# Optimization experiments

Measured on AMD Instinct MI355X. Metric: run time of the kernel, lower is better.

Reference implementation:

```python
import jax, jax.numpy as jnp
import numpy as np

N_NODES = 100000
N_EDGES = 1600000
N_GRAPHS = 2000
IN_DIM = 37
HID = 128
OUT_CLS = 2


def _leconv(x, src, dst, w, W1, b1, W2, W3, b3):
    # PyG LEConv: out[i] = sum_j w_ij * (lin1(x)[i] - lin2(x)[j]) + lin3(x)[i]
    a = x @ W1 + b1          # [N, H]
    b = x @ W2               # [N, H] (lin2 has no bias)
    c = x @ W3 + b3          # [N, H]
    deg = jax.ops.segment_sum(w, dst, num_segments=N_NODES)              # [N]
    agg = jax.ops.segment_sum(w[:, None] * b[src], dst, num_segments=N_NODES)  # [N, H]
    return deg[:, None] * a - agg + c


def setup_inputs() -> dict:
    key = jax.random.key(0)
    ks = jax.random.split(key, 32)
    inp = {}
    inp["x"] = jax.random.normal(ks[0], (N_NODES, IN_DIM), dtype=jnp.float32)
    inp["edge_index"] = jax.random.randint(ks[1], (2, N_EDGES), 0, N_NODES, dtype=jnp.int64)
    inp["batch"] = jnp.sort(jax.random.randint(ks[2], (N_NODES,), 0, N_GRAPHS, dtype=jnp.int64))
    dims = [(IN_DIM, HID), (HID, HID), (HID, HID)]
    ki = 3
    for l, (di, do) in enumerate(dims):
        s = 1.0 / np.sqrt(di)
        inp[f"W1_{l}"] = jax.random.uniform(ks[ki + 0], (di, do), jnp.float32, -s, s)
        inp[f"b1_{l}"] = jax.random.uniform(ks[ki + 1], (do,), jnp.float32, -s, s)
        inp[f"W2_{l}"] = jax.random.uniform(ks[ki + 2], (di, do), jnp.float32, -s, s)
        inp[f"W3_{l}"] = jax.random.uniform(ks[ki + 3], (di, do), jnp.float32, -s, s)
        inp[f"b3_{l}"] = jax.random.uniform(ks[ki + 4], (do,), jnp.float32, -s, s)
        ki += 5
    sf = 1.0 / np.sqrt(HID)
    inp["Wf1"] = jax.random.uniform(ks[ki + 0], (HID, HID), jnp.float32, -sf, sf)
    inp["bf1"] = jax.random.uniform(ks[ki + 1], (HID,), jnp.float32, -sf, sf)
    inp["Wf2"] = jax.random.uniform(ks[ki + 2], (HID, OUT_CLS), jnp.float32, -sf, sf)
    inp["bf2"] = jax.random.uniform(ks[ki + 3], (OUT_CLS,), jnp.float32, -sf, sf)
    return inp


def reference(x, edge_index, batch,
              W1_0, b1_0, W2_0, W3_0, b3_0,
              W1_1, b1_1, W2_1, W3_1, b3_1,
              W1_2, b1_2, W2_2, W3_2, b3_2,
              Wf1, bf1, Wf2, bf2):
    src, dst = edge_index[0], edge_index[1]
    w = jnp.ones((edge_index.shape[1],), dtype=x.dtype)  # edge_weight = ones
    layers = [(W1_0, b1_0, W2_0, W3_0, b3_0),
              (W1_1, b1_1, W2_1, W3_1, b3_1),
              (W1_2, b1_2, W2_2, W3_2, b3_2)]
    h = x
    for (W1, b1, W2, W3, b3) in layers:
        h = jax.nn.relu(_leconv(h, src, dst, w, W1, b1, W2, W3, b3))
    # global mean pool per graph
    sums = jax.ops.segment_sum(h, batch, num_segments=N_GRAPHS)           # [G, H]
    cnt = jax.ops.segment_sum(jnp.ones((N_NODES,), h.dtype), batch, num_segments=N_GRAPHS)
    graph_x = sums / jnp.clip(cnt, 1.0)[:, None]
    # FFN head (Dropout is identity at inference)
    pred = jax.nn.relu(graph_x @ Wf1 + bf1) @ Wf2 + bf2                   # [G, 2]
    return pred
```

## Files before the change

### kernel.cpp

```cpp
#include <hip/hip_runtime.h>
#include <hip/hip_bf16.h>
#include <cstdint>

#define N_NODES 100000
#define N_EDGES 1600000
#define N_GRAPHS 2000
#define IN_DIM 37
#define HID 128

#define GEMM_GRID 1563
#define HIST_BLOCKS 6250
#define PACK67_BLOCKS 384
#define PREPACK_BLOCKS 96

typedef __attribute__((ext_vector_type(8))) short short8;
typedef __attribute__((ext_vector_type(4))) float f32x4;

static __device__ __forceinline__ short bf16_bits(float f) {
    __hip_bfloat16 h = __float2bfloat16(f);
    return *reinterpret_cast<short*>(&h);
}
static __device__ __forceinline__ float bf16_lo(uint32_t u) {
    uint32_t v = u << 16;
    return *reinterpret_cast<float*>(&v);
}
static __device__ __forceinline__ float bf16_hi(uint32_t u) {
    uint32_t v = u & 0xffff0000u;
    return *reinterpret_cast<float*>(&v);
}


struct PackArgs {
    const float* w[9];
    short* o[9];
};

static __device__ __forceinline__ void pack_one(const PackArgs& pa, int m, int r, int kin) {
    const int i = r & 7, lane = (r >> 3) & 63, t = (r >> 9) & 7, kb = r >> 12;
    const int k = kb * 32 + (lane >> 4) * 8 + i;
    const int c = t * 16 + (lane & 15);
    float v = (k < kin) ? pa.w[m][(size_t)k * HID + c] : 0.f;
    pa.o[m][r] = bf16_bits(v);
}

__global__ __launch_bounds__(256) void prepack_kernel(PackArgs pa) {
    const int idx = blockIdx.x * 256 + threadIdx.x;
    pack_one(pa, idx >> 13, idx & 8191, IN_DIM);
}


static __device__ __forceinline__ void gemm0_body(
    int blk, const float* __restrict__ x,
    const short* __restrict__ Wp1, const short* __restrict__ Wp2, const short* __restrict__ Wp3,
    const float* __restrict__ b1v, const float* __restrict__ b3v,
    short* __restrict__ D0, short* __restrict__ E0, short* __restrict__ Bb) {
    const int tid = threadIdx.x;
    const int wave = tid >> 6, lane = tid & 63;
    const int row_base = blk * 64 + wave * 16;
    const int r15 = lane & 15, kg = lane >> 4;
    int arow = row_base + r15;
    if (arow >= N_NODES) arow = N_NODES - 1;
    const float* xr = x + (size_t)arow * IN_DIM;

    f32x4 acc1[8], acc2[8], acc3[8];
    #pragma unroll
    for (int t = 0; t < 8; t++) {
        acc1[t] = (f32x4)0.f; acc2[t] = (f32x4)0.f; acc3[t] = (f32x4)0.f;
    }
    #pragma unroll
    for (int kb = 0; kb < 2; kb++) {
        short8 av;
        #pragma unroll
        for (int i = 0; i < 8; i++) {
            const int k = kb * 32 + kg * 8 + i;
            av[i] = (k < IN_DIM) ? bf16_bits(xr[k]) : (short)0;
        }
        #pragma unroll
        for (int t = 0; t < 8; t++) {
            const int widx = (kb * 8 + t) * 512 + lane * 8;
            short8 w1 = *(const short8*)(Wp1 + widx);
            short8 w2 = *(const short8*)(Wp2 + widx);
            short8 w3 = *(const short8*)(Wp3 + widx);
            acc1[t] = __builtin_amdgcn_mfma_f32_16x16x32_bf16(av, w1, acc1[t], 0, 0, 0);
            acc2[t] = __builtin_amdgcn_mfma_f32_16x16x32_bf16(av, w2, acc2[t], 0, 0, 0);
            acc3[t] = __builtin_amdgcn_mfma_f32_16x16x32_bf16(av, w3, acc3[t], 0, 0, 0);
        }
    }
    int grow[4]; bool ok[4];
    #pragma unroll
    for (int i = 0; i < 4; i++) {
        grow[i] = row_base + kg * 4 + i;
        ok[i] = grow[i] < N_NODES;
    }
    #pragma unroll
    for (int t = 0; t < 8; t++) {
        const int c = t * 16 + r15;
        const float bb1 = b1v[c], bb3 = b3v[c];
        #pragma unroll
        for (int i = 0; i < 4; i++) {
            if (ok[i]) {
                size_t o = (size_t)grow[i] * HID + c;
                D0[o] = bf16_bits(acc1[t][i] + bb1);
                E0[o] = bf16_bits(acc3[t][i] + bb3);
                Bb[o] = bf16_bits(acc2[t][i]);
            }
        }
    }
}


struct P1Args {
    const float* x;
    const int* ei;
    int* cnt; int* rank;
    const short* Wp1; const short* Wp2; const short* Wp3;
    const float* b1; const float* b3;
    short* D0; short* E0; short* Bb;
    PackArgs pa;
};

__global__ __launch_bounds__(256) void phase1_kernel(P1Args a) {
    const int b = blockIdx.x;
    if (b < GEMM_GRID) {
        gemm0_body(b, a.x, a.Wp1, a.Wp2, a.Wp3, a.b1, a.b3, a.D0, a.E0, a.Bb);
        return;
    }
    if (b < GEMM_GRID + HIST_BLOCKS) {
        const int e = (b - GEMM_GRID) * 256 + threadIdx.x;
        const int d = a.ei[N_EDGES + e];
        a.rank[e] = atomicAdd(&a.cnt[d], 1);
        return;
    }
    const int idx = (b - GEMM_GRID - HIST_BLOCKS) * 256 + threadIdx.x;
    pack_one(a.pa, 3 + (idx >> 14), idx & 16383, HID);
}


__global__ __launch_bounds__(1024) void scan_blocks(const int* __restrict__ cnt,
                                                    int* __restrict__ partial,
                                                    int* __restrict__ bsum) {
    __shared__ int ws[16];
    const int tid = threadIdx.x, lane = tid & 63, wv = tid >> 6;
    const int i = blockIdx.x * 1024 + tid;
    int v0 = (i < N_NODES) ? cnt[i] : 0;
    int v = v0;
    #pragma unroll
    for (int off = 1; off < 64; off <<= 1) {
        int n = __shfl_up(v, off, 64);
        if (lane >= off) v += n;
    }
    if (lane == 63) ws[wv] = v;
    __syncthreads();
    int woff = 0, tot = 0;
    #pragma unroll
    for (int w = 0; w < 16; w++) {
        int s = ws[w];
        if (w < wv) woff += s;
        tot += s;
    }
    if (i < N_NODES) partial[i] = woff + v - v0;
    if (tid == 0) bsum[blockIdx.x] = tot;
}

__global__ __launch_bounds__(1024) void scan_finalize(const int* __restrict__ partial,
                                                      const int* __restrict__ bsum,
                                                      const int* __restrict__ cnt,
                                                      int* __restrict__ rowptr,
                                                      float* __restrict__ degf) {
    __shared__ int off_s;
    const int tid = threadIdx.x, b = blockIdx.x;
    if (tid < 64) {
        int acc = 0;
        for (int j = tid; j < b; j += 64) acc += bsum[j];
        #pragma unroll
        for (int off = 32; off; off >>= 1) acc += __shfl_down(acc, off, 64);
        if (tid == 0) off_s = acc;
    }
    __syncthreads();
    const int i = b * 1024 + tid;
    if (i < N_NODES) {
        rowptr[i] = off_s + partial[i];
        degf[i] = (float)cnt[i];
    }
    if (b == 0 && tid == 0) rowptr[N_NODES] = N_EDGES;
}


__global__ __launch_bounds__(256) void fill_kernel(const int* __restrict__ ei,
                                                   const int* __restrict__ rank,
                                                   const int* __restrict__ rowptr,
                                                   int* __restrict__ col) {
    const int e = blockIdx.x * 256 + threadIdx.x;
    const int s = ei[e];
    const int d = ei[N_EDGES + e];
    col[rowptr[d] + rank[e]] = s;
}


static __device__ __forceinline__ void agg_edges(const int* __restrict__ col, int s, int e,
                                                 const short* __restrict__ Bb, int lane2,
                                                 float& AX, float& AY) {
    float ax0 = 0.f, ay0 = 0.f, ax1 = 0.f, ay1 = 0.f;
    int t = s;
    for (; t < e && (t & 3); t++) {
        const uint32_t u = *(const uint32_t*)(Bb + (size_t)col[t] * HID + lane2);
        ax0 += bf16_lo(u); ay0 += bf16_hi(u);
    }
    for (; t + 4 <= e; t += 4) {
        const int4 c4 = *(const int4*)(col + t);
        const uint32_t u0 = *(const uint32_t*)(Bb + (size_t)c4.x * HID + lane2);
        const uint32_t u1 = *(const uint32_t*)(Bb + (size_t)c4.y * HID + lane2);
        const uint32_t u2 = *(const uint32_t*)(Bb + (size_t)c4.z * HID + lane2);
        const uint32_t u3 = *(const uint32_t*)(Bb + (size_t)c4.w * HID + lane2);
        ax0 += bf16_lo(u0) + bf16_lo(u2);
        ay0 += bf16_hi(u0) + bf16_hi(u2);
        ax1 += bf16_lo(u1) + bf16_lo(u3);
        ay1 += bf16_hi(u1) + bf16_hi(u3);
    }
    for (; t < e; t++) {
        const uint32_t u = *(const uint32_t*)(Bb + (size_t)col[t] * HID + lane2);
        ax0 += bf16_lo(u); ay0 += bf16_hi(u);
    }
    AX = ax0 + ax1; AY = ay0 + ay1;
}

__global__ __launch_bounds__(256) void gather0_kernel(const int* __restrict__ rowptr,
                                                      const int* __restrict__ col,
                                                      const short* __restrict__ Bb,
                                                      const short* __restrict__ D0,
                                                      const short* __restrict__ E0,
                                                      short* __restrict__ Hb) {
    const int wid = (blockIdx.x * 256 + threadIdx.x) >> 6;
    const int lane2 = (threadIdx.x & 63) * 2;
    if (wid >= N_NODES) return;
    const int s = rowptr[wid], e = rowptr[wid + 1];
    float ax, ay;
    agg_edges(col, s, e, Bb, lane2, ax, ay);
    const float dg = (float)(e - s);
    const uint32_t ud = *(const uint32_t*)(D0 + (size_t)wid * HID + lane2);
    const uint32_t ue = *(const uint32_t*)(E0 + (size_t)wid * HID + lane2);
    const float ox = fmaxf(fmaf(dg, bf16_lo(ud), bf16_lo(ue)) - ax, 0.f);
    const float oy = fmaxf(fmaf(dg, bf16_hi(ud), bf16_hi(ue)) - ay, 0.f);
    *(uint32_t*)(Hb + (size_t)wid * HID + lane2) =
        ((uint32_t)(uint16_t)bf16_bits(oy) << 16) | (uint16_t)bf16_bits(ox);
}

__global__ __launch_bounds__(256) void gatherL_kernel(const int* __restrict__ rowptr,
                                                      const int* __restrict__ col,
                                                      const short* __restrict__ Bb,
                                                      const short* __restrict__ OUTb,
                                                      short* __restrict__ Hb) {
    const int wid = (blockIdx.x * 256 + threadIdx.x) >> 6;
    const int lane2 = (threadIdx.x & 63) * 2;
    if (wid >= N_NODES) return;
    const int s = rowptr[wid], e = rowptr[wid + 1];
    float ax, ay;
    agg_edges(col, s, e, Bb, lane2, ax, ay);
    const uint32_t uo = *(const uint32_t*)(OUTb + (size_t)wid * HID + lane2);
    const float ox = fmaxf(bf16_lo(uo) - ax, 0.f);
    const float oy = fmaxf(bf16_hi(uo) - ay, 0.f);
    *(uint32_t*)(Hb + (size_t)wid * HID + lane2) =
        ((uint32_t)(uint16_t)bf16_bits(oy) << 16) | (uint16_t)bf16_bits(ox);
}


__global__ __launch_bounds__(256) void leconv_mfma(
    const short* __restrict__ Hb,
    const short* __restrict__ Wp1, const short* __restrict__ Wp2, const short* __restrict__ Wp3,
    const float* __restrict__ b1v, const float* __restrict__ b3v,
    const float* __restrict__ deg,
    short* __restrict__ Bb, short* __restrict__ OUTb) {
    const int tid = threadIdx.x;
    const int wave = tid >> 6, lane = tid & 63;
    const int row_base = blockIdx.x * 64 + wave * 16;
    const int r15 = lane & 15, kg = lane >> 4;
    int arow = row_base + r15;
    if (arow >= N_NODES) arow = N_NODES - 1;
    const short* aptr = Hb + (size_t)arow * HID + kg * 8;

    f32x4 acc1[8], acc2[8], acc3[8];
    #pragma unroll
    for (int t = 0; t < 8; t++) {
        acc1[t] = (f32x4)0.f; acc2[t] = (f32x4)0.f; acc3[t] = (f32x4)0.f;
    }
    #pragma unroll
    for (int kb = 0; kb < 4; kb++) {
        short8 av = *(const short8*)(aptr + kb * 32);
        #pragma unroll
        for (int t = 0; t < 8; t++) {
            const int widx = (kb * 8 + t) * 512 + lane * 8;
            short8 w1 = *(const short8*)(Wp1 + widx);
            short8 w2 = *(const short8*)(Wp2 + widx);
            short8 w3 = *(const short8*)(Wp3 + widx);
            acc1[t] = __builtin_amdgcn_mfma_f32_16x16x32_bf16(av, w1, acc1[t], 0, 0, 0);
            acc2[t] = __builtin_amdgcn_mfma_f32_16x16x32_bf16(av, w2, acc2[t], 0, 0, 0);
            acc3[t] = __builtin_amdgcn_mfma_f32_16x16x32_bf16(av, w3, acc3[t], 0, 0, 0);
        }
    }
    int grow[4]; bool ok[4]; float dg[4];
    #pragma unroll
    for (int i = 0; i < 4; i++) {
        grow[i] = row_base + kg * 4 + i;
        ok[i] = grow[i] < N_NODES;
        dg[i] = ok[i] ? deg[grow[i]] : 0.f;
    }
    #pragma unroll
    for (int t = 0; t < 8; t++) {
        const int c = t * 16 + r15;
        const float bb1 = b1v[c], bb3 = b3v[c];
        #pragma unroll
        for (int i = 0; i < 4; i++) {
            if (ok[i]) {
                size_t o = (size_t)grow[i] * HID + c;
                OUTb[o] = bf16_bits(dg[i] * (acc1[t][i] + bb1) + acc3[t][i] + bb3);
                Bb[o] = bf16_bits(acc2[t][i]);
            }
        }
    }
}


__global__ __launch_bounds__(128) void pool_ffn_kernel(const short* __restrict__ H,
                                                       const int* __restrict__ batch,
                                                       const float* __restrict__ Wf1,
                                                       const float* __restrict__ bf1,
                                                       const float* __restrict__ Wf2,
                                                       const float* __restrict__ bf2,
                                                       float* __restrict__ out) {
    const int g = blockIdx.x;
    const int t = threadIdx.x;

    int lo = 0, hi = N_NODES;
    while (lo < hi) { int mid = (lo + hi) >> 1; if (batch[mid] < g) lo = mid + 1; else hi = mid; }
    const int s = lo;
    hi = N_NODES;
    while (lo < hi) { int mid = (lo + hi) >> 1; if (batch[mid] < g + 1) lo = mid + 1; else hi = mid; }
    const int e = lo;

    float sum = 0.f;
    for (int n = s; n < e; n++) {
        short b = H[(size_t)n * HID + t];
        sum += __bfloat162float(*(__hip_bfloat16*)&b);
    }
    const float cntf = (float)(e - s);
    const float gx = sum / fmaxf(cntf, 1.f);

    __shared__ float lds[HID];
    lds[t] = gx;
    __syncthreads();

    float hsum = bf1[t];
    #pragma unroll 8
    for (int k = 0; k < HID; k++) hsum = fmaf(lds[k], Wf1[k * HID + t], hsum);
    const float hr = fmaxf(hsum, 0.f);

    float p0 = hr * Wf2[t * 2 + 0];
    float p1 = hr * Wf2[t * 2 + 1];
    #pragma unroll
    for (int off = 32; off > 0; off >>= 1) {
        p0 += __shfl_down(p0, off, 64);
        p1 += __shfl_down(p1, off, 64);
    }
    __shared__ float red[4];
    if ((t & 63) == 0) {
        red[(t >> 6) * 2 + 0] = p0;
        red[(t >> 6) * 2 + 1] = p1;
    }
    __syncthreads();
    if (t == 0) {
        out[g * 2 + 0] = red[0] + red[2] + bf2[0];
        out[g * 2 + 1] = red[1] + red[3] + bf2[1];
    }
}


extern "C" void kernel_launch(void* const* d_in, const int* in_sizes, int n_in,
                              void* d_out, int out_size, void* d_ws, size_t ws_size,
                              hipStream_t stream) {
    (void)in_sizes; (void)n_in; (void)out_size; (void)ws_size;

    const float* x     = (const float*)d_in[0];
    const int*   ei    = (const int*)d_in[1];
    const int*   batch = (const int*)d_in[2];
    const float* W[9] = {
        (const float*)d_in[3],  (const float*)d_in[5],  (const float*)d_in[6],
        (const float*)d_in[8],  (const float*)d_in[10], (const float*)d_in[11],
        (const float*)d_in[13], (const float*)d_in[15], (const float*)d_in[16]};
    const float* b1_0 = (const float*)d_in[4];
    const float* b3_0 = (const float*)d_in[7];
    const float* b1_1 = (const float*)d_in[9];
    const float* b3_1 = (const float*)d_in[12];
    const float* b1_2 = (const float*)d_in[14];
    const float* b3_2 = (const float*)d_in[17];
    const float* Wf1  = (const float*)d_in[18];
    const float* bf1  = (const float*)d_in[19];
    const float* Wf2  = (const float*)d_in[20];
    const float* bf2  = (const float*)d_in[21];
    float* out = (float*)d_out;

    char* ws = (char*)d_ws;
    size_t off = 0;
    auto alloc = [&](size_t bytes) {
        void* p = ws + off;
        off += (bytes + 255) & ~(size_t)255;
        return p;
    };
    short* D0     = (short*)alloc((size_t)N_NODES * HID * 2);
    short* E0     = (short*)alloc((size_t)N_NODES * HID * 2);
    short* Bb_A   = (short*)alloc((size_t)N_NODES * HID * 2);
    short* Bb_B   = (short*)alloc((size_t)N_NODES * HID * 2);
    short* Hb     = (short*)alloc((size_t)N_NODES * HID * 2);
    float* degf   = (float*)alloc((size_t)N_NODES * 4);
    int*   rowptr = (int*)alloc((size_t)(N_NODES + 1) * 4);
    int*   cnt    = (int*)alloc((size_t)N_NODES * 4);
    int*   col    = (int*)alloc((size_t)N_EDGES * 4);
    int*   rank   = (int*)alloc((size_t)N_EDGES * 4);
    int*   partial= (int*)alloc((size_t)N_NODES * 4);
    int*   bsum   = (int*)alloc(1024);
    short* P[9];
    for (int m = 0; m < 9; m++) P[m] = (short*)alloc(16384 * 2);

    hipMemsetAsync(cnt, 0, (size_t)N_NODES * 4, stream);

    PackArgs pa;
    for (int m = 0; m < 9; m++) { pa.w[m] = W[m]; pa.o[m] = P[m]; }

    prepack_kernel<<<PREPACK_BLOCKS, 256, 0, stream>>>(pa);

    P1Args p1{ x, ei, cnt, rank, P[0], P[1], P[2], b1_0, b3_0, D0, E0, Bb_A, pa };
    phase1_kernel<<<GEMM_GRID + HIST_BLOCKS + PACK67_BLOCKS, 256, 0, stream>>>(p1);

    const int NSB = (N_NODES + 1023) / 1024;
    scan_blocks<<<NSB, 1024, 0, stream>>>(cnt, partial, bsum);
    scan_finalize<<<NSB, 1024, 0, stream>>>(partial, bsum, cnt, rowptr, degf);

    fill_kernel<<<HIST_BLOCKS, 256, 0, stream>>>(ei, rank, rowptr, col);

    const int gather_grid = (N_NODES * 64 + 255) / 256;

    gather0_kernel<<<gather_grid, 256, 0, stream>>>(rowptr, col, Bb_A, D0, E0, Hb);
    leconv_mfma<<<GEMM_GRID, 256, 0, stream>>>(Hb, P[3], P[4], P[5], b1_1, b3_1, degf, Bb_B, E0);
    gatherL_kernel<<<gather_grid, 256, 0, stream>>>(rowptr, col, Bb_B, E0, Hb);
    leconv_mfma<<<GEMM_GRID, 256, 0, stream>>>(Hb, P[6], P[7], P[8], b1_2, b3_2, degf, Bb_A, D0);
    gatherL_kernel<<<gather_grid, 256, 0, stream>>>(rowptr, col, Bb_A, D0, Hb);

    pool_ffn_kernel<<<N_GRAPHS, 128, 0, stream>>>(Hb, batch, Wf1, bf1, Wf2, bf2, out);
}
```

Baseline: 526.5 us.

## Split gather wave into four edge groups with 16-byte row loads

```diff
diff --git a/kernel.cpp b/kernel.cpp
--- a/kernel.cpp
+++ b/kernel.cpp
@@ -27,6 +27,9 @@
 static __device__ __forceinline__ float bf16_hi(uint32_t u) {
     uint32_t v = u & 0xffff0000u;
     return *reinterpret_cast<float*>(&v);
+}
+static __device__ __forceinline__ uint32_t pack_bf16(float lo, float hi) {
+    return ((uint32_t)(uint16_t)bf16_bits(hi) << 16) | (uint16_t)bf16_bits(lo);
 }
 
 
@@ -197,31 +200,34 @@
 }
 
 
-static __device__ __forceinline__ void agg_edges(const int* __restrict__ col, int s, int e,
-                                                 const short* __restrict__ Bb, int lane2,
-                                                 float& AX, float& AY) {
-    float ax0 = 0.f, ay0 = 0.f, ax1 = 0.f, ay1 = 0.f;
-    int t = s;
-    for (; t < e && (t & 3); t++) {
-        const uint32_t u = *(const uint32_t*)(Bb + (size_t)col[t] * HID + lane2);
-        ax0 += bf16_lo(u); ay0 += bf16_hi(u);
-    }
-    for (; t + 4 <= e; t += 4) {
-        const int4 c4 = *(const int4*)(col + t);
-        const uint32_t u0 = *(const uint32_t*)(Bb + (size_t)c4.x * HID + lane2);
-        const uint32_t u1 = *(const uint32_t*)(Bb + (size_t)c4.y * HID + lane2);
-        const uint32_t u2 = *(const uint32_t*)(Bb + (size_t)c4.z * HID + lane2);
-        const uint32_t u3 = *(const uint32_t*)(Bb + (size_t)c4.w * HID + lane2);
-        ax0 += bf16_lo(u0) + bf16_lo(u2);
-        ay0 += bf16_hi(u0) + bf16_hi(u2);
-        ax1 += bf16_lo(u1) + bf16_lo(u3);
-        ay1 += bf16_hi(u1) + bf16_hi(u3);
-    }
-    for (; t < e; t++) {
-        const uint32_t u = *(const uint32_t*)(Bb + (size_t)col[t] * HID + lane2);
-        ax0 += bf16_lo(u); ay0 += bf16_hi(u);
-    }
-    AX = ax0 + ax1; AY = ay0 + ay1;
+static __device__ __forceinline__ void agg_edges4(const int* __restrict__ col, int s, int e,
+                                                  const short* __restrict__ Bb,
+                                                  int lane, int grp, int l16, float* acc) {
+    for (int base = s; base < e; base += 64) {
+        const int cnt = min(64, e - base);
+        const int ci = base + lane;
+        const int cv = col[(ci < e) ? ci : (e - 1)];
+        for (int t = 0; t < cnt; t += 4) {
+            const int idx = t + grp;
+            const bool on = idx < cnt;
+            const float w = on ? 1.f : 0.f;
+            const int c = __shfl(cv, on ? idx : 0, 64);
+            const uint4 u = *(const uint4*)(Bb + (size_t)c * HID + l16 * 8);
+            acc[0] = fmaf(w, bf16_lo(u.x), acc[0]);
+            acc[1] = fmaf(w, bf16_hi(u.x), acc[1]);
+            acc[2] = fmaf(w, bf16_lo(u.y), acc[2]);
+            acc[3] = fmaf(w, bf16_hi(u.y), acc[3]);
+            acc[4] = fmaf(w, bf16_lo(u.z), acc[4]);
+            acc[5] = fmaf(w, bf16_hi(u.z), acc[5]);
+            acc[6] = fmaf(w, bf16_lo(u.w), acc[6]);
+            acc[7] = fmaf(w, bf16_hi(u.w), acc[7]);
+        }
+    }
+    #pragma unroll
+    for (int j = 0; j < 8; j++) {
+        acc[j] += __shfl_xor(acc[j], 16, 64);
+        acc[j] += __shfl_xor(acc[j], 32, 64);
+    }
 }
 
 __global__ __launch_bounds__(256) void gather0_kernel(const int* __restrict__ rowptr,
@@ -231,18 +237,26 @@
                                                       const short* __restrict__ E0,
                                                       short* __restrict__ Hb) {
     const int wid = (blockIdx.x * 256 + threadIdx.x) >> 6;
-    const int lane2 = (threadIdx.x & 63) * 2;
     if (wid >= N_NODES) return;
+    const int lane = threadIdx.x & 63, grp = lane >> 4, l16 = lane & 15;
     const int s = rowptr[wid], e = rowptr[wid + 1];
-    float ax, ay;
-    agg_edges(col, s, e, Bb, lane2, ax, ay);
-    const float dg = (float)(e - s);
-    const uint32_t ud = *(const uint32_t*)(D0 + (size_t)wid * HID + lane2);
-    const uint32_t ue = *(const uint32_t*)(E0 + (size_t)wid * HID + lane2);
-    const float ox = fmaxf(fmaf(dg, bf16_lo(ud), bf16_lo(ue)) - ax, 0.f);
-    const float oy = fmaxf(fmaf(dg, bf16_hi(ud), bf16_hi(ue)) - ay, 0.f);
-    *(uint32_t*)(Hb + (size_t)wid * HID + lane2) =
-        ((uint32_t)(uint16_t)bf16_bits(oy) << 16) | (uint16_t)bf16_bits(ox);
+    float acc[8] = {0.f, 0.f, 0.f, 0.f, 0.f, 0.f, 0.f, 0.f};
+    agg_edges4(col, s, e, Bb, lane, grp, l16, acc);
+    if (grp == 0) {
+        const float dg = (float)(e - s);
+        const uint4 ud = *(const uint4*)(D0 + (size_t)wid * HID + l16 * 8);
+        const uint4 ue = *(const uint4*)(E0 + (size_t)wid * HID + l16 * 8);
+        uint4 r;
+        r.x = pack_bf16(fmaxf(fmaf(dg, bf16_lo(ud.x), bf16_lo(ue.x)) - acc[0], 0.f),
+                        fmaxf(fmaf(dg, bf16_hi(ud.x), bf16_hi(ue.x)) - acc[1], 0.f));
+        r.y = pack_bf16(fmaxf(fmaf(dg, bf16_lo(ud.y), bf16_lo(ue.y)) - acc[2], 0.f),
+                        fmaxf(fmaf(dg, bf16_hi(ud.y), bf16_hi(ue.y)) - acc[3], 0.f));
+        r.z = pack_bf16(fmaxf(fmaf(dg, bf16_lo(ud.z), bf16_lo(ue.z)) - acc[4], 0.f),
+                        fmaxf(fmaf(dg, bf16_hi(ud.z), bf16_hi(ue.z)) - acc[5], 0.f));
+        r.w = pack_bf16(fmaxf(fmaf(dg, bf16_lo(ud.w), bf16_lo(ue.w)) - acc[6], 0.f),
+                        fmaxf(fmaf(dg, bf16_hi(ud.w), bf16_hi(ue.w)) - acc[7], 0.f));
+        *(uint4*)(Hb + (size_t)wid * HID + l16 * 8) = r;
+    }
 }
 
 __global__ __launch_bounds__(256) void gatherL_kernel(const int* __restrict__ rowptr,
@@ -251,16 +265,20 @@
                                                       const short* __restrict__ OUTb,
                                                       short* __restrict__ Hb) {
     const int wid = (blockIdx.x * 256 + threadIdx.x) >> 6;
-    const int lane2 = (threadIdx.x & 63) * 2;
     if (wid >= N_NODES) return;
+    const int lane = threadIdx.x & 63, grp = lane >> 4, l16 = lane & 15;
     const int s = rowptr[wid], e = rowptr[wid + 1];
-    float ax, ay;
-    agg_edges(col, s, e, Bb, lane2, ax, ay);
-    const uint32_t uo = *(const uint32_t*)(OUTb + (size_t)wid * HID + lane2);
-    const float ox = fmaxf(bf16_lo(uo) - ax, 0.f);
-    const float oy = fmaxf(bf16_hi(uo) - ay, 0.f);
-    *(uint32_t*)(Hb + (size_t)wid * HID + lane2) =
-        ((uint32_t)(uint16_t)bf16_bits(oy) << 16) | (uint16_t)bf16_bits(ox);
+    float acc[8] = {0.f, 0.f, 0.f, 0.f, 0.f, 0.f, 0.f, 0.f};
+    agg_edges4(col, s, e, Bb, lane, grp, l16, acc);
+    if (grp == 0) {
+        const uint4 uo = *(const uint4*)(OUTb + (size_t)wid * HID + l16 * 8);
+        uint4 r;
+        r.x = pack_bf16(fmaxf(bf16_lo(uo.x) - acc[0], 0.f), fmaxf(bf16_hi(uo.x) - acc[1], 0.f));
+        r.y = pack_bf16(fmaxf(bf16_lo(uo.y) - acc[2], 0.f), fmaxf(bf16_hi(uo.y) - acc[3], 0.f));
+        r.z = pack_bf16(fmaxf(bf16_lo(uo.z) - acc[4], 0.f), fmaxf(bf16_hi(uo.z) - acc[5], 0.f));
+        r.w = pack_bf16(fmaxf(bf16_lo(uo.w) - acc[6], 0.f), fmaxf(bf16_hi(uo.w) - acc[7], 0.f));
+        *(uint4*)(Hb + (size_t)wid * HID + l16 * 8) = r;
+    }
 }
 
 
```

Measured after the change: 475.3 us. 1.11x faster.
